# Performance work log

Hardware: AMD Instinct MI355X
Metric: run time of the kernel (lower is better)

Reference implementation:

```python
import jax, jax.numpy as jnp
import numpy as np


def conv2d(x, w, b, stride=1, pad=1):
    y = jax.lax.conv_general_dilated(
        x, w, (stride, stride), [(pad, pad), (pad, pad)],
        dimension_numbers=('NCHW', 'OIHW', 'NCHW'))
    return y + b[None, :, None, None]


def layernorm(x, g, b, eps=1e-5):
    mu = jnp.mean(x, -1, keepdims=True)
    var = jnp.mean((x - mu) ** 2, -1, keepdims=True)
    return (x - mu) * jax.lax.rsqrt(var + eps) * g + b


def setup_inputs() -> dict:
    key = jax.random.key(0)
    ks = iter(jax.random.split(key, 40))
    nf = 4

    def w(shape, scale=0.1):
        return (jax.random.normal(next(ks), shape, jnp.float32) * scale)

    inp = {}
    inp['x'] = jax.random.uniform(next(ks), (8, 3, 512, 512), jnp.float32)
    # curve-estimation convs (channel=4)
    inp['c1_w'], inp['c1_b'] = w((nf, 1, 3, 3)), w((nf,))
    inp['c2_w'], inp['c2_b'] = w((nf, nf, 3, 3)), w((nf,))
    inp['c3_w'], inp['c3_b'] = w((nf, nf, 3, 3)), w((nf,))
    inp['c4_w'], inp['c4_b'] = w((nf, nf, 3, 3)), w((nf,))
    inp['c5_w'], inp['c5_b'] = w((nf, 2 * nf, 3, 3)), w((nf,))
    inp['c6_w'], inp['c6_b'] = w((nf, 2 * nf, 3, 3)), w((nf,))
    inp['c7_w'], inp['c7_b'] = w((1, 2 * nf, 3, 3)), w((1,))
    # global branch: conv 1->16 stride 2, instance norm (affine)
    inp['m_w'], inp['m_b'] = w((16, 1, 3, 3)), w((16,))
    inp['in_g'] = jnp.ones((16,), jnp.float32)
    inp['in_b'] = jnp.zeros((16,), jnp.float32)
    # TF block (d_model=16, nhead=8, dim_ff=128), eval mode (no dropout)
    inp['attn_w'], inp['attn_b'] = w((48, 16)), w((48,))
    inp['out_w'], inp['out_b'] = w((16, 16)), w((16,))
    inp['l1_w'], inp['l1_b'] = w((128, 16)), w((128,))
    inp['l2_w'], inp['l2_b'] = w((16, 128)), w((16,))
    inp['n1_g'] = jnp.ones((16,), jnp.float32)
    inp['n1_b'] = jnp.zeros((16,), jnp.float32)
    inp['n2_g'] = jnp.ones((16,), jnp.float32)
    inp['n2_b'] = jnp.zeros((16,), jnp.float32)
    # F: Conv2d(16, 2, kernel=16, pad=0) over 16x16 -> [B,2,1,1]
    inp['f_w'], inp['f_b'] = w((2, 16, 16, 16)), w((2,))
    return inp


def _forward(x, c1_w, c1_b, c2_w, c2_b, c3_w, c3_b, c4_w, c4_b, c5_w, c5_b,
             c6_w, c6_b, c7_w, c7_b, m_w, m_b, in_g, in_b, attn_w, attn_b,
             out_w, out_b, l1_w, l1_b, l2_w, l2_b, n1_g, n1_b, n2_g, n2_b,
             f_w, f_b):
    relu = jax.nn.relu
    B, _, H, W = x.shape
    red, green, blue = x[:, 0:1], x[:, 1:2], x[:, 2:3]
    v = (red + green + blue) / 3.0  # [B,1,H,W]

    # curve-estimation branch
    x1 = relu(conv2d(v, c1_w, c1_b))
    x2 = relu(conv2d(x1, c2_w, c2_b))
    x3 = relu(conv2d(x2, c3_w, c3_b))
    x4 = relu(conv2d(x3, c4_w, c4_b))
    x5 = relu(conv2d(jnp.concatenate([x3, x4], 1), c5_w, c5_b))
    x6 = relu(conv2d(jnp.concatenate([x2, x5], 1), c6_w, c6_b))
    v_r = jax.nn.sigmoid(conv2d(jnp.concatenate([x1, x6], 1), c7_w, c7_b))

    # where(v>0.999999, 0.999999, .) ; where(v<1e-6, 1e-6, .)  == clip
    v0 = jnp.clip(v, 1e-6, 0.999999)

    # nearest-neighbor resize to 32x32 (torch 'nearest': floor(i * src/dst))
    idx_h = (jnp.arange(32) * H) // 32
    idx_w = (jnp.arange(32) * W) // 32
    v32 = v[:, :, idx_h][:, :, :, idx_w]  # [B,1,32,32]

    # model: conv stride2 -> leaky relu -> instance norm (affine)
    h = conv2d(v32, m_w, m_b, stride=2, pad=1)  # [B,16,16,16]
    h = jnp.where(h >= 0, h, 0.2 * h)
    mu = jnp.mean(h, (2, 3), keepdims=True)
    var = jnp.mean((h - mu) ** 2, (2, 3), keepdims=True)
    v1 = (h - mu) * jax.lax.rsqrt(var + 1e-5)
    v1 = v1 * in_g[None, :, None, None] + in_b[None, :, None, None]

    # TF block on [S=256, B, E=16] tokens, 8 heads of dim 2, eval mode
    bb, cc, ww, hh = v1.shape
    src = v1.reshape(bb, cc, ww * hh).transpose(2, 0, 1)  # [S,B,E]
    S, E, nH = ww * hh, cc, 8
    hd = E // nH
    qkv = src @ attn_w.T + attn_b  # [S,B,3E]
    q, k, vv = jnp.split(qkv, 3, axis=-1)
    q = q.reshape(S, bb, nH, hd)
    k = k.reshape(S, bb, nH, hd)
    vv = vv.reshape(S, bb, nH, hd)
    scores = jnp.einsum('sbhd,tbhd->bhst', q, k) / np.sqrt(hd).astype(np.float32)
    attn = jax.nn.softmax(scores, axis=-1)
    o = jnp.einsum('bhst,tbhd->sbhd', attn, vv).reshape(S, bb, E)
    o = o @ out_w.T + out_b
    src = layernorm(src + o, n1_g, n1_b)
    ff = jax.nn.relu(src @ l1_w.T + l1_b) @ l2_w.T + l2_b
    src = layernorm(src + ff, n2_g, n2_b)
    v5 = src.transpose(1, 2, 0).reshape(bb, cc, ww, hh)

    level = jax.nn.sigmoid(conv2d(v5, f_w, f_b, stride=1, pad=0))[:, :, 0, 0]  # [B,2]

    # per-sample exponent / threshold broadcast (vectorized .item() loop)
    g = (0.1 * level[:, 0] + 0.2)[:, None, None, None]   # [B,1,1,1]
    bcf = (0.04 * level[:, 1] + 0.06)[:, None, None, None]
    r0 = jnp.power(g, v_r)           # g ** r, elementwise per sample
    ev0 = jnp.power(v0, r0)
    L = 400.0 * (bcf - v) ** 3
    L = jnp.where(L < 1e-5, 1e-6, L)
    ev = ev0 - L
    vd = v + 1e-6
    enhance = jnp.concatenate([red / vd * ev, green / vd * ev, blue / vd * ev], 1)
    vvv = jnp.concatenate([v, v, v], 1)
    t = jnp.where(vvv > 0.04, jnp.zeros_like(enhance), enhance)
    return enhance, v_r, t


def reference(x, c1_w, c1_b, c2_w, c2_b, c3_w, c3_b, c4_w, c4_b, c5_w, c5_b,
              c6_w, c6_b, c7_w, c7_b, m_w, m_b, in_g, in_b, attn_w, attn_b,
              out_w, out_b, l1_w, l1_b, l2_w, l2_b, n1_g, n1_b, n2_g, n2_b,
              f_w, f_b):
    return _forward(x, c1_w, c1_b, c2_w, c2_b, c3_w, c3_b, c4_w, c4_b,
                    c5_w, c5_b, c6_w, c6_b, c7_w, c7_b, m_w, m_b, in_g, in_b,
                    attn_w, attn_b, out_w, out_b, l1_w, l1_b, l2_w, l2_b,
                    n1_g, n1_b, n2_g, n2_b, f_w, f_b)
```

## Files before the change

kernel.cpp:

```cpp
#include <hip/hip_runtime.h>
#include <math.h>

#define H 512
#define W 512
#define PLANE (H*W)
#define PLANE4 (PLANE/4)

typedef unsigned int uint;
typedef unsigned short ushort;
typedef _Float16 h2 __attribute__((ext_vector_type(2)));

__device__ __forceinline__ h2 bch2(uint u){ return __builtin_bit_cast(h2, u); }
__device__ __forceinline__ uint pkf16(float a, float b){
  return __builtin_bit_cast(uint, __builtin_amdgcn_cvt_pkrtz(a, b));
}

#define LOADWIN_EVEN(WIN, TL, S, YB, XB) { \
  _Pragma("unroll") for (int r_=0;r_<4;++r_){ \
    uint4 Ua = *(const uint4*)&(TL)[(((YB)+r_)*(S)+(XB))*4]; \
    uint4 Ub = *(const uint4*)&(TL)[(((YB)+r_)*(S)+(XB)+2)*4]; \
    WIN[r_][0][0]=bch2(Ua.x); WIN[r_][0][1]=bch2(Ua.y); \
    WIN[r_][1][0]=bch2(Ua.z); WIN[r_][1][1]=bch2(Ua.w); \
    WIN[r_][2][0]=bch2(Ub.x); WIN[r_][2][1]=bch2(Ub.y); \
    WIN[r_][3][0]=bch2(Ub.z); WIN[r_][3][1]=bch2(Ub.w); } }

#define LOADWIN_ODD(WIN, TL, S, YB, XB) { \
  _Pragma("unroll") for (int r_=0;r_<4;++r_){ \
    uint2 U0 = *(const uint2*)&(TL)[(((YB)+r_)*(S)+(XB))*4]; \
    uint4 U1 = *(const uint4*)&(TL)[(((YB)+r_)*(S)+(XB)+1)*4]; \
    uint2 U2 = *(const uint2*)&(TL)[(((YB)+r_)*(S)+(XB)+3)*4]; \
    WIN[r_][0][0]=bch2(U0.x); WIN[r_][0][1]=bch2(U0.y); \
    WIN[r_][1][0]=bch2(U1.x); WIN[r_][1][1]=bch2(U1.y); \
    WIN[r_][2][0]=bch2(U1.z); WIN[r_][2][1]=bch2(U1.w); \
    WIN[r_][3][0]=bch2(U2.x); WIN[r_][3][1]=bch2(U2.y); } }

#define DOTACC(WIN, WPK, NPTOT, PBASE, NPWIN) { \
  _Pragma("unroll") for (int p_=0;p_<NPWIN;++p_){ \
    _Pragma("unroll") for (int dy_=0;dy_<3;++dy_){ \
      _Pragma("unroll") for (int dx_=0;dx_<3;++dx_){ \
        h2 aa=WIN[dy_][dx_][p_],   bb=WIN[dy_][dx_+1][p_]; \
        h2 cc=WIN[dy_+1][dx_][p_], dd=WIN[dy_+1][dx_+1][p_]; \
        _Pragma("unroll") for (int co_=0;co_<4;++co_){ \
          h2 wv = bch2((WPK)[((co_*(NPTOT))+(PBASE)+p_)*9+dy_*3+dx_]); \
          a00[co_]=__builtin_amdgcn_fdot2(aa,wv,a00[co_],false); \
          a01[co_]=__builtin_amdgcn_fdot2(bb,wv,a01[co_],false); \
          a10[co_]=__builtin_amdgcn_fdot2(cc,wv,a10[co_],false); \
          a11[co_]=__builtin_amdgcn_fdot2(dd,wv,a11[co_],false); } } } } }

#define DOTACC1(WIN, WPK, PBASE) { \
  _Pragma("unroll") for (int p_=0;p_<2;++p_){ \
    _Pragma("unroll") for (int dy_=0;dy_<3;++dy_){ \
      _Pragma("unroll") for (int dx_=0;dx_<3;++dx_){ \
        h2 wv = bch2((WPK)[((PBASE)+p_)*9+dy_*3+dx_]); \
        s00=__builtin_amdgcn_fdot2(WIN[dy_][dx_][p_],  wv,s00,false); \
        s01=__builtin_amdgcn_fdot2(WIN[dy_][dx_+1][p_],wv,s01,false); \
        s10=__builtin_amdgcn_fdot2(WIN[dy_+1][dx_][p_],  wv,s10,false); \
        s11=__builtin_amdgcn_fdot2(WIN[dy_+1][dx_+1][p_],wv,s11,false); } } } }

#define STORE_TILE(TL, S, GOFF) { \
    bool okr0=(unsigned)(gy0+(GOFF)+y0  )<512u; \
    bool okr1=(unsigned)(gy0+(GOFF)+y0+1)<512u; \
    bool okc0=(unsigned)(gx0+(GOFF)+x0  )<512u; \
    bool okc1=(unsigned)(gx0+(GOFF)+x0+1)<512u; \
    float v00[4],v01[4],v10[4],v11[4]; \
    _Pragma("unroll") \
    for (int co_=0;co_<4;++co_){ \
      v00[co_]=(okr0&okc0)?fmaxf(a00[co_],0.f):0.f; \
      v01[co_]=(okr0&okc1)?fmaxf(a01[co_],0.f):0.f; \
      v10[co_]=(okr1&okc0)?fmaxf(a10[co_],0.f):0.f; \
      v11[co_]=(okr1&okc1)?fmaxf(a11[co_],0.f):0.f; } \
    uint4 rowlo, rowhi; \
    rowlo.x=pkf16(v00[0],v00[1]); rowlo.y=pkf16(v00[2],v00[3]); \
    rowlo.z=pkf16(v01[0],v01[1]); rowlo.w=pkf16(v01[2],v01[3]); \
    rowhi.x=pkf16(v10[0],v10[1]); rowhi.y=pkf16(v10[2],v10[3]); \
    rowhi.z=pkf16(v11[0],v11[1]); rowhi.w=pkf16(v11[2],v11[3]); \
    *(uint4*)&(TL)[(y0*(S)+x0)*4]=rowlo; \
    *(uint4*)&(TL)[((y0+1)*(S)+x0)*4]=rowhi; }

template<int S>
__device__ __forceinline__ void accp4sc(const ushort* __restrict__ pl,
    const float* __restrict__ w, int YB, int XB,
    float* a00, float* a01, float* a10, float* a11)
{
  float q[4][4];
  #pragma unroll
  for (int r=0;r<4;++r){
    const ushort* rp = pl + (YB+r)*S + XB;
    h2 p0 = bch2(*(const uint*)rp);
    h2 p1 = bch2(*(const uint*)(rp+2));
    q[r][0]=(float)p0.x; q[r][1]=(float)p0.y; q[r][2]=(float)p1.x; q[r][3]=(float)p1.y;
  }
  #pragma unroll
  for (int dy=0; dy<3; ++dy)
    #pragma unroll
    for (int dx=0; dx<3; ++dx){
      float q00=q[dy][dx], q01=q[dy][dx+1], q10=q[dy+1][dx], q11=q[dy+1][dx+1];
      #pragma unroll
      for (int co=0; co<4; ++co){
        float wv=w[co*9+dy*3+dx];
        a00[co]+=q00*wv; a01[co]+=q01*wv; a10[co]+=q10*wv; a11[co]+=q11*wv;
      }
    }
}

__global__ void k_wprep(const float* __restrict__ c2w, const float* __restrict__ c3w,
                        const float* __restrict__ c4w, const float* __restrict__ c5w,
                        const float* __restrict__ c6w, const float* __restrict__ c7w,
                        uint* __restrict__ wpk){
  for (int i=threadIdx.x; i<540; i+=512){
    const float* src; int INC, rel;
    if (i<72){src=c2w;INC=4;rel=i;}
    else if (i<144){src=c3w;INC=4;rel=i-72;}
    else if (i<216){src=c4w;INC=4;rel=i-144;}
    else if (i<360){src=c5w;INC=8;rel=i-216;}
    else if (i<504){src=c6w;INC=8;rel=i-360;}
    else {src=c7w;INC=8;rel=i-504;}
    int NP=INC/2;
    int co=rel/(NP*9); int r2=rel-co*NP*9; int p=r2/9; int tap=r2-p*9;
    float f0 = src[(co*INC + 2*p  )*9 + tap];
    float f1 = src[(co*INC + 2*p+1)*9 + tap];
    wpk[i] = pkf16(f0, f1);
  }
}

__launch_bounds__(512,2)
__global__ void k_megaconv(const float* __restrict__ xg,
    const float* __restrict__ c1w, const float* __restrict__ c1b,
    const float* __restrict__ c2b, const float* __restrict__ c3b,
    const float* __restrict__ c4b, const float* __restrict__ c5b,
    const float* __restrict__ c6b, const float* __restrict__ c7b,
    const uint* __restrict__ wpk,
    float* __restrict__ vr)
{
  __shared__ __align__(16) ushort vb[46*46];
  __shared__ __align__(16) ushort t1[44*44*4];
  __shared__ __align__(16) ushort t2[42*42*4];
  __shared__ __align__(16) ushort t3[40*40*4];
  __shared__ __align__(16) ushort t4[38*38*4];
  __shared__ __align__(16) ushort t5[36*36*4];
  __shared__ __align__(16) ushort t6[34*34*4];
  int wg=blockIdx.x, b=wg>>8, t=wg&255, ty=t>>4, tx=t&15;
  int gy0=ty*32, gx0=tx*32, tid=threadIdx.x;
  const float* xp = xg + (size_t)b*3*PLANE;

  for (int i=tid;i<46*46;i+=512){
    int rr=i/46, cc=i-rr*46;
    int gy=gy0-7+rr, gx=gx0-7+cc;
    float val=0.f;
    if (((unsigned)gy<512u)&((unsigned)gx<512u)){
      int off=gy*W+gx;
      val=(xp[off]+xp[PLANE+off]+xp[2*PLANE+off])*(1.f/3.f);
    }
    _Float16 hv=(_Float16)val;
    vb[i]=*(ushort*)&hv;
  }
  __syncthreads();

  if (tid < 484){
    int qy=tid/22, qx=tid-qy*22, y0=2*qy, x0=2*qx;
    float a00[4],a01[4],a10[4],a11[4];
    #pragma unroll
    for (int co=0;co<4;++co){ float bv=c1b[co]; a00[co]=bv;a01[co]=bv;a10[co]=bv;a11[co]=bv; }
    accp4sc<46>(vb, c1w, y0, x0, a00,a01,a10,a11);
    STORE_TILE(t1, 44, -6)
  }
  __syncthreads();

  if (tid < 441){
    int qy=tid/21, qx=tid-qy*21, y0=2*qy, x0=2*qx;
    float a00[4],a01[4],a10[4],a11[4];
    #pragma unroll
    for (int co=0;co<4;++co){ float bv=c2b[co]; a00[co]=bv;a01[co]=bv;a10[co]=bv;a11[co]=bv; }
    h2 win[4][4][2];
    LOADWIN_EVEN(win, t1, 44, y0, x0)
    DOTACC(win, wpk+0, 2, 0, 2)
    STORE_TILE(t2, 42, -5)
  }
  __syncthreads();

  if (tid < 400){
    int qy=tid/20, qx=tid-qy*20, y0=2*qy, x0=2*qx;
    float a00[4],a01[4],a10[4],a11[4];
    #pragma unroll
    for (int co=0;co<4;++co){ float bv=c3b[co]; a00[co]=bv;a01[co]=bv;a10[co]=bv;a11[co]=bv; }
    h2 win[4][4][2];
    LOADWIN_EVEN(win, t2, 42, y0, x0)
    DOTACC(win, wpk+72, 2, 0, 2)
    STORE_TILE(t3, 40, -4)
  }
  __syncthreads();

  if (tid < 361){
    int qy=tid/19, qx=tid-qy*19, y0=2*qy, x0=2*qx;
    float a00[4],a01[4],a10[4],a11[4];
    #pragma unroll
    for (int co=0;co<4;++co){ float bv=c4b[co]; a00[co]=bv;a01[co]=bv;a10[co]=bv;a11[co]=bv; }
    h2 win[4][4][2];
    LOADWIN_EVEN(win, t3, 40, y0, x0)
    DOTACC(win, wpk+144, 2, 0, 2)
    STORE_TILE(t4, 38, -3)
  }
  __syncthreads();

  if (tid < 324){
    int qy=tid/18, qx=tid-qy*18, y0=2*qy, x0=2*qx;
    float a00[4],a01[4],a10[4],a11[4];
    #pragma unroll
    for (int co=0;co<4;++co){ float bv=c5b[co]; a00[co]=bv;a01[co]=bv;a10[co]=bv;a11[co]=bv; }
    {
      h2 win[4][4][2];
      LOADWIN_ODD(win, t3, 40, y0+1, x0+1)
      DOTACC(win, wpk+216, 4, 0, 2)
    }
    {
      h2 win[4][4][2];
      LOADWIN_EVEN(win, t4, 38, y0, x0)
      DOTACC(win, wpk+216, 4, 2, 2)
    }
    STORE_TILE(t5, 36, -2)
  }
  __syncthreads();

  if (tid < 289){
    int qy=tid/17, qx=tid-qy*17, y0=2*qy, x0=2*qx;
    float a00[4],a01[4],a10[4],a11[4];
    #pragma unroll
    for (int co=0;co<4;++co){ float bv=c6b[co]; a00[co]=bv;a01[co]=bv;a10[co]=bv;a11[co]=bv; }
    {
      h2 win[4][4][2];
      LOADWIN_ODD(win, t2, 42, y0+3, x0+3)
      DOTACC(win, wpk+360, 4, 0, 2)
    }
    {
      h2 win[4][4][2];
      LOADWIN_EVEN(win, t5, 36, y0, x0)
      DOTACC(win, wpk+360, 4, 2, 2)
    }
    STORE_TILE(t6, 34, -1)
  }
  __syncthreads();

  if (tid < 256){
    int qy=tid>>4, qx=tid&15, y0=2*qy, x0=2*qx;
    float bv=c7b[0];
    float s00=bv, s01=bv, s10=bv, s11=bv;
    {
      h2 win[4][4][2];
      LOADWIN_ODD(win, t1, 44, y0+5, x0+5)
      DOTACC1(win, wpk+504, 0)
    }
    {
      h2 win[4][4][2];
      LOADWIN_EVEN(win, t6, 34, y0, x0)
      DOTACC1(win, wpk+504, 2)
    }
    float* vo = vr + (size_t)b*PLANE;
    *(float2*)&vo[(gy0+y0  )*512 + gx0+x0] =
        make_float2(1.f/(1.f+expf(-s00)), 1.f/(1.f+expf(-s01)));
    *(float2*)&vo[(gy0+y0+1)*512 + gx0+x0] =
        make_float2(1.f/(1.f+expf(-s10)), 1.f/(1.f+expf(-s11)));
  }
}

__launch_bounds__(256)
__global__ void k_mnorm(const float* __restrict__ xg, const float* __restrict__ mw,
                        const float* __restrict__ mb, const float* __restrict__ ing,
                        const float* __restrict__ inb, float* __restrict__ src){
  int bc = blockIdx.x;
  int b = bc >> 4, c = bc & 15;
  int tid = threadIdx.x;
  int i = tid >> 4, j = tid & 15;
  const float* xp = xg + (size_t)b*3*PLANE;
  float s = mb[c];
  #pragma unroll
  for (int dy=0; dy<3; ++dy){
    int ii = 2*i - 1 + dy;
    if ((unsigned)ii >= 32u) continue;
    #pragma unroll
    for (int dx=0; dx<3; ++dx){
      int jj = 2*j - 1 + dx;
      if ((unsigned)jj >= 32u) continue;
      int off = (ii*16)*W + jj*16;
      float vv = (xp[off] + xp[PLANE+off] + xp[2*PLANE+off]) * (1.f/3.f);
      s += vv * mw[c*9 + dy*3 + dx];
    }
  }
  float h = (s >= 0.f) ? s : 0.2f*s;
  __shared__ float red[256];
  red[tid] = h; __syncthreads();
  for (int off=128; off; off>>=1){ if (tid<off) red[tid]+=red[tid+off]; __syncthreads(); }
  float mu = red[0] * (1.f/256.f);
  __syncthreads();
  float d = h - mu;
  red[tid] = d*d; __syncthreads();
  for (int off=128; off; off>>=1){ if (tid<off) red[tid]+=red[tid+off]; __syncthreads(); }
  float var = red[0] * (1.f/256.f);
  float yv = d * rsqrtf(var + 1e-5f) * ing[c] + inb[c];
  src[(size_t)tid*128 + b*16 + c] = yv;
}

__launch_bounds__(256)
__global__ void k_qkv(const float* __restrict__ src, const float* __restrict__ aw,
                      const float* __restrict__ ab, float* __restrict__ qkv){
  int id = blockIdx.x*256 + threadIdx.x;
  int tok = id / 48, o = id % 48;
  const float* sr = src + tok*16;
  float s = ab[o];
  #pragma unroll
  for (int e=0; e<16; ++e) s += sr[e]*aw[o*16+e];
  qkv[tok*48+o] = s;
}

__launch_bounds__(256)
__global__ void k_attn(const float* __restrict__ qkv, float* __restrict__ obuf){
  int b = blockIdx.x >> 3, hh = blockIdx.x & 7;
  int t = threadIdx.x;
  __shared__ float kk0[256], kk1[256], vv0[256], vv1[256];
  int tok = t*8 + b;
  const float* qr = qkv + tok*48;
  kk0[t] = qr[16 + hh*2]; kk1[t] = qr[16 + hh*2 + 1];
  vv0[t] = qr[32 + hh*2]; vv1[t] = qr[32 + hh*2 + 1];
  float q0 = qr[hh*2], q1 = qr[hh*2 + 1];
  __syncthreads();
  const float sc = 0.70710678118654752f;
  float m = -1e30f;
  for (int u=0; u<256; ++u){
    float s = (q0*kk0[u] + q1*kk1[u]) * sc;
    m = fmaxf(m, s);
  }
  float l = 0.f, a0 = 0.f, a1 = 0.f;
  for (int u=0; u<256; ++u){
    float s = (q0*kk0[u] + q1*kk1[u]) * sc;
    float p = expf(s - m);
    l += p; a0 += p*vv0[u]; a1 += p*vv1[u];
  }
  float inv = 1.f/l;
  obuf[tok*16 + hh*2]     = a0*inv;
  obuf[tok*16 + hh*2 + 1] = a1*inv;
}

__launch_bounds__(256)
__global__ void k_oproj_ln(const float* __restrict__ obuf, const float* __restrict__ ow,
                           const float* __restrict__ obias, const float* __restrict__ g,
                           const float* __restrict__ bb, float* __restrict__ src){
  int tok = blockIdx.x*256 + threadIdx.x;
  const float* orow = obuf + tok*16;
  float xv[16];
  #pragma unroll
  for (int e=0; e<16; ++e){
    float s = obias[e];
    #pragma unroll
    for (int f=0; f<16; ++f) s += orow[f]*ow[e*16+f];
    xv[e] = src[tok*16+e] + s;
  }
  float mu = 0.f;
  #pragma unroll
  for (int e=0; e<16; ++e) mu += xv[e];
  mu *= (1.f/16.f);
  float var = 0.f;
  #pragma unroll
  for (int e=0; e<16; ++e){ float d = xv[e]-mu; var += d*d; }
  var *= (1.f/16.f);
  float rs = rsqrtf(var + 1e-5f);
  #pragma unroll
  for (int e=0; e<16; ++e) src[tok*16+e] = (xv[e]-mu)*rs*g[e] + bb[e];
}

__launch_bounds__(64)
__global__ void k_ffn_ln(float* __restrict__ src, const float* __restrict__ w1,
                         const float* __restrict__ b1, const float* __restrict__ w2,
                         const float* __restrict__ b2, const float* __restrict__ g,
                         const float* __restrict__ bb){
  int tok = blockIdx.x;
  int tid = threadIdx.x;
  __shared__ float srow[16], h1[128], xr[16];
  if (tid < 16) srow[tid] = src[tok*16+tid];
  __syncthreads();
  for (int i = tid; i < 128; i += 64){
    float s = b1[i];
    #pragma unroll
    for (int e=0; e<16; ++e) s += srow[e]*w1[i*16+e];
    h1[i] = fmaxf(s, 0.f);
  }
  __syncthreads();
  if (tid < 16){
    float s = b2[tid];
    for (int j=0; j<128; ++j) s += h1[j]*w2[tid*128+j];
    xr[tid] = srow[tid] + s;
  }
  __syncthreads();
  if (tid < 16){
    float mu = 0.f;
    #pragma unroll
    for (int e=0; e<16; ++e) mu += xr[e];
    mu *= (1.f/16.f);
    float var = 0.f;
    #pragma unroll
    for (int e=0; e<16; ++e){ float d = xr[e]-mu; var += d*d; }
    var *= (1.f/16.f);
    src[tok*16+tid] = (xr[tid]-mu)*rsqrtf(var+1e-5f)*g[tid] + bb[tid];
  }
}

__launch_bounds__(256)
__global__ void k_level(const float* __restrict__ src, const float* __restrict__ fw,
                        const float* __restrict__ fb, float* __restrict__ gb){
  int b = blockIdx.x >> 1, k = blockIdx.x & 1;
  int tid = threadIdx.x;
  float s = 0.f;
  #pragma unroll
  for (int c=0; c<16; ++c)
    s += src[(size_t)tid*128 + b*16 + c] * fw[(k*16+c)*256 + tid];
  __shared__ float red[256];
  red[tid] = s; __syncthreads();
  for (int off=128; off; off>>=1){ if (tid<off) red[tid]+=red[tid+off]; __syncthreads(); }
  if (tid == 0){
    float lev = 1.f/(1.f + expf(-(red[0] + fb[k])));
    gb[b*2+k] = (k==0) ? (0.1f*lev + 0.2f) : (0.04f*lev + 0.06f);
  }
}

__launch_bounds__(256)
__global__ void k_final(const float* __restrict__ x, const float* __restrict__ gb,
                        float* __restrict__ out){
  int id = blockIdx.x*256 + threadIdx.x;
  int b = id >> 16, p = id & 65535;
  const float4* xr = (const float4*)(x + (size_t)(b*3+0)*PLANE);
  const float4* xg = (const float4*)(x + (size_t)(b*3+1)*PLANE);
  const float4* xb = (const float4*)(x + (size_t)(b*3+2)*PLANE);
  const float4* vrp = (const float4*)(out + 6291456 + (size_t)b*PLANE);
  float4 R = xr[p], G = xg[p], Bl = xb[p], VR = vrp[p];
  float gg = gb[b*2+0], bc = gb[b*2+1];
  float lg = log2f(gg);
  float4 er, eg, eb, tr, tg, tb;
#define COMP(SUF, RF, GF, BF, VRF) {            \
    float vv = (RF + GF + BF)/3.f;              \
    float v0 = fminf(fmaxf(vv, 1e-6f), 0.999999f); \
    float r0 = exp2f(VRF * lg);                 \
    float ev0 = exp2f(r0 * log2f(v0));          \
    float d = bc - vv;                          \
    float L = 400.f*d*d*d;                      \
    L = (L < 1e-5f) ? 1e-6f : L;                \
    float fac = (ev0 - L) / (vv + 1e-6f);       \
    er.SUF = RF*fac; eg.SUF = GF*fac; eb.SUF = BF*fac; \
    bool z = vv > 0.04f;                        \
    tr.SUF = z ? 0.f : er.SUF; tg.SUF = z ? 0.f : eg.SUF; tb.SUF = z ? 0.f : eb.SUF; }
  COMP(x, R.x, G.x, Bl.x, VR.x)
  COMP(y, R.y, G.y, Bl.y, VR.y)
  COMP(z, R.z, G.z, Bl.z, VR.z)
  COMP(w, R.w, G.w, Bl.w, VR.w)
#undef COMP
  float4* oe = (float4*)out;
  float4* ot = (float4*)(out + 8388608);
  oe[(size_t)(b*3+0)*PLANE4 + p] = er;
  oe[(size_t)(b*3+1)*PLANE4 + p] = eg;
  oe[(size_t)(b*3+2)*PLANE4 + p] = eb;
  ot[(size_t)(b*3+0)*PLANE4 + p] = tr;
  ot[(size_t)(b*3+1)*PLANE4 + p] = tg;
  ot[(size_t)(b*3+2)*PLANE4 + p] = tb;
}

extern "C" void kernel_launch(void* const* d_in, const int* in_sizes, int n_in,
                              void* d_out, int out_size, void* d_ws, size_t ws_size,
                              hipStream_t stream) {
  const float* x    = (const float*)d_in[0];
  const float* c1w  = (const float*)d_in[1];  const float* c1b = (const float*)d_in[2];
  const float* c2w  = (const float*)d_in[3];  const float* c2b = (const float*)d_in[4];
  const float* c3w  = (const float*)d_in[5];  const float* c3b = (const float*)d_in[6];
  const float* c4w  = (const float*)d_in[7];  const float* c4b = (const float*)d_in[8];
  const float* c5w  = (const float*)d_in[9];  const float* c5b = (const float*)d_in[10];
  const float* c6w  = (const float*)d_in[11]; const float* c6b = (const float*)d_in[12];
  const float* c7w  = (const float*)d_in[13]; const float* c7b = (const float*)d_in[14];
  const float* mw   = (const float*)d_in[15]; const float* mb  = (const float*)d_in[16];
  const float* ing  = (const float*)d_in[17]; const float* inb = (const float*)d_in[18];
  const float* aw   = (const float*)d_in[19]; const float* ab  = (const float*)d_in[20];
  const float* ow   = (const float*)d_in[21]; const float* ob  = (const float*)d_in[22];
  const float* l1w  = (const float*)d_in[23]; const float* l1b = (const float*)d_in[24];
  const float* l2w  = (const float*)d_in[25]; const float* l2b = (const float*)d_in[26];
  const float* n1g  = (const float*)d_in[27]; const float* n1b = (const float*)d_in[28];
  const float* n2g  = (const float*)d_in[29]; const float* n2b = (const float*)d_in[30];
  const float* fw   = (const float*)d_in[31]; const float* fb  = (const float*)d_in[32];

  uint* wpk = (uint*)d_ws;
  float* smallws = (float*)(wpk + 1024);
  float* src  = smallws;
  float* qkv  = src + 32768;
  float* obuf = qkv + 98304;
  float* gb   = obuf+ 32768;
  float* out  = (float*)d_out;
  float* vr   = out + 6291456;

  k_wprep<<<1,512,0,stream>>>(c2w, c3w, c4w, c5w, c6w, c7w, wpk);
  k_megaconv<<<2048,512,0,stream>>>(x, c1w, c1b, c2b, c3b, c4b, c5b, c6b, c7b,
                                    wpk, vr);
  k_mnorm<<<128,256,0,stream>>>(x, mw, mb, ing, inb, src);
  k_qkv<<<384,256,0,stream>>>(src, aw, ab, qkv);
  k_attn<<<64,256,0,stream>>>(qkv, obuf);
  k_oproj_ln<<<8,256,0,stream>>>(obuf, ow, ob, n1g, n1b, src);
  k_ffn_ln<<<2048,64,0,stream>>>(src, l1w, l1b, l2w, l2b, n2g, n2b);
  k_level<<<16,256,0,stream>>>(src, fw, fb, gb);
  k_final<<<2048,256,0,stream>>>(x, gb, out);
}
```

Baseline: 167.3 us.

## Fuse transformer branch into one kernel and fold final enhancement into megaconv

The global branch (instance norm, QKV, attention, out-projection with layernorm, FFN with layernorm, level head) was six small kernels. It is now one kernel, `k_small`, with one block per batch and all intermediates kept in shared memory; attention also drops the running-max subtraction. That kernel now runs before the conv kernel, so the conv epilogue can apply the curve enhancement directly and write both outputs. This removes the separate final pass over the image and the extra re-read of the stored v_r map, plus several launches. The cost is that the small branch now runs serially on only 8 blocks before the big conv kernel, and the conv epilogue gets heavier.

```diff
diff --git a/kernel.cpp b/kernel.cpp
--- a/kernel.cpp
+++ b/kernel.cpp
@@ -123,14 +123,190 @@
   }
 }
 
+__launch_bounds__(256)
+__global__ void k_small(const float* __restrict__ xg,
+    const float* __restrict__ mw, const float* __restrict__ mb,
+    const float* __restrict__ ing, const float* __restrict__ inb,
+    const float* __restrict__ aw, const float* __restrict__ ab,
+    const float* __restrict__ ow, const float* __restrict__ ob,
+    const float* __restrict__ l1w, const float* __restrict__ l1b,
+    const float* __restrict__ l2w, const float* __restrict__ l2b,
+    const float* __restrict__ n1g, const float* __restrict__ n1b,
+    const float* __restrict__ n2g, const float* __restrict__ n2b,
+    const float* __restrict__ fw, const float* __restrict__ fb,
+    float* __restrict__ gb)
+{
+  __shared__ float srcl[256][17];
+  __shared__ float qkvl[256][49];
+  __shared__ float obufl[256][17];
+  __shared__ float red[512];
+  __shared__ float musig[32];
+  int b = blockIdx.x, tid = threadIdx.x;
+  int i = tid>>4, j = tid&15;
+  const float* xp = xg + (size_t)b*3*PLANE;
+
+  float vs[3][3];
+  #pragma unroll
+  for (int dy=0;dy<3;++dy){
+    int ii = 2*i-1+dy;
+    #pragma unroll
+    for (int dx=0;dx<3;++dx){
+      int jj = 2*j-1+dx;
+      float v = 0.f;
+      if (((unsigned)ii<32u)&((unsigned)jj<32u)){
+        int off = (ii*16)*W + jj*16;
+        v = (xp[off]+xp[PLANE+off]+xp[2*PLANE+off])*(1.f/3.f);
+      }
+      vs[dy][dx]=v;
+    }
+  }
+  float h[16];
+  #pragma unroll
+  for (int c=0;c<16;++c){
+    float s = mb[c];
+    #pragma unroll
+    for (int dy=0;dy<3;++dy)
+      #pragma unroll
+      for (int dx=0;dx<3;++dx) s += vs[dy][dx]*mw[c*9+dy*3+dx];
+    h[c] = (s>=0.f)?s:0.2f*s;
+    srcl[tid][c]=h[c];
+  }
+  __syncthreads();
+  {
+    int c = tid>>4, g = tid&15;
+    float s1=0.f, s2=0.f;
+    #pragma unroll
+    for (int p=0;p<16;++p){ float v=srcl[g*16+p][c]; s1+=v; s2+=v*v; }
+    red[c*16+g]=s1; red[256+c*16+g]=s2;
+  }
+  __syncthreads();
+  if (tid<16){
+    float S1=0.f,S2=0.f;
+    #pragma unroll
+    for (int g=0;g<16;++g){ S1+=red[tid*16+g]; S2+=red[256+tid*16+g]; }
+    float mu=S1*(1.f/256.f);
+    float var=S2*(1.f/256.f)-mu*mu;
+    musig[tid]=mu; musig[16+tid]=rsqrtf(var+1e-5f);
+  }
+  __syncthreads();
+  #pragma unroll
+  for (int c=0;c<16;++c)
+    srcl[tid][c] = (h[c]-musig[c])*musig[16+c]*ing[c]+inb[c];
+  __syncthreads();
+
+  {
+    float s[16];
+    #pragma unroll
+    for (int e=0;e<16;++e) s[e]=srcl[tid][e];
+    for (int o=0;o<48;++o){
+      float t = ab[o];
+      #pragma unroll
+      for (int e=0;e<16;++e) t += s[e]*aw[o*16+e];
+      qkvl[tid][o]=t;
+    }
+  }
+  __syncthreads();
+
+  {
+    const float sc = 0.70710678118654752f;
+    #pragma unroll
+    for (int hh=0;hh<8;++hh){
+      float q0=qkvl[tid][2*hh], q1=qkvl[tid][2*hh+1];
+      float l=0.f,a0=0.f,a1=0.f;
+      for (int u=0;u<256;++u){
+        float k0=qkvl[u][16+2*hh], k1=qkvl[u][16+2*hh+1];
+        float p=expf((q0*k0+q1*k1)*sc);
+        l+=p; a0+=p*qkvl[u][32+2*hh]; a1+=p*qkvl[u][32+2*hh+1];
+      }
+      float inv=1.f/l;
+      obufl[tid][2*hh]=a0*inv; obufl[tid][2*hh+1]=a1*inv;
+    }
+  }
+  __syncthreads();
+
+  {
+    float xv[16];
+    #pragma unroll
+    for (int e=0;e<16;++e){
+      float t=ob[e];
+      #pragma unroll
+      for (int f=0;f<16;++f) t += obufl[tid][f]*ow[e*16+f];
+      xv[e]=srcl[tid][e]+t;
+    }
+    float mu=0.f;
+    #pragma unroll
+    for (int e=0;e<16;++e) mu+=xv[e];
+    mu*=(1.f/16.f);
+    float var=0.f;
+    #pragma unroll
+    for (int e=0;e<16;++e){ float d=xv[e]-mu; var+=d*d; }
+    var*=(1.f/16.f);
+    float rs=rsqrtf(var+1e-5f);
+    #pragma unroll
+    for (int e=0;e<16;++e) srcl[tid][e]=(xv[e]-mu)*rs*n1g[e]+n1b[e];
+  }
+  __syncthreads();
+
+  {
+    float s[16], x2[16];
+    #pragma unroll
+    for (int e=0;e<16;++e){ s[e]=srcl[tid][e]; x2[e]=l2b[e]; }
+    for (int ii2=0;ii2<128;++ii2){
+      float t=l1b[ii2];
+      #pragma unroll
+      for (int e=0;e<16;++e) t += s[e]*l1w[ii2*16+e];
+      t = fmaxf(t,0.f);
+      #pragma unroll
+      for (int e=0;e<16;++e) x2[e] += t*l2w[e*128+ii2];
+    }
+    float xv[16];
+    #pragma unroll
+    for (int e=0;e<16;++e) xv[e]=s[e]+x2[e];
+    float mu=0.f;
+    #pragma unroll
+    for (int e=0;e<16;++e) mu+=xv[e];
+    mu*=(1.f/16.f);
+    float var=0.f;
+    #pragma unroll
+    for (int e=0;e<16;++e){ float d=xv[e]-mu; var+=d*d; }
+    var*=(1.f/16.f);
+    float rs=rsqrtf(var+1e-5f);
+    #pragma unroll
+    for (int e=0;e<16;++e) srcl[tid][e]=(xv[e]-mu)*rs*n2g[e]+n2b[e];
+  }
+  __syncthreads();
+
+  {
+    float p0=0.f,p1=0.f;
+    #pragma unroll
+    for (int c=0;c<16;++c){
+      float sv=srcl[tid][c];
+      p0 += sv*fw[c*256+tid];
+      p1 += sv*fw[(16+c)*256+tid];
+    }
+    red[tid]=p0; red[256+tid]=p1;
+  }
+  __syncthreads();
+  for (int off=128; off; off>>=1){
+    if (tid<off){ red[tid]+=red[tid+off]; red[256+tid]+=red[256+tid+off]; }
+    __syncthreads();
+  }
+  if (tid==0){
+    float lev0 = 1.f/(1.f+expf(-(red[0]+fb[0])));
+    float lev1 = 1.f/(1.f+expf(-(red[256]+fb[1])));
+    gb[b*2+0] = 0.1f*lev0+0.2f;
+    gb[b*2+1] = 0.04f*lev1+0.06f;
+  }
+}
+
 __launch_bounds__(512,2)
 __global__ void k_megaconv(const float* __restrict__ xg,
     const float* __restrict__ c1w, const float* __restrict__ c1b,
     const float* __restrict__ c2b, const float* __restrict__ c3b,
     const float* __restrict__ c4b, const float* __restrict__ c5b,
     const float* __restrict__ c6b, const float* __restrict__ c7b,
-    const uint* __restrict__ wpk,
-    float* __restrict__ vr)
+    const uint* __restrict__ wpk, const float* __restrict__ gb2,
+    float* __restrict__ out)
 {
   __shared__ __align__(16) ushort vb[46*46];
   __shared__ __align__(16) ushort t1[44*44*4];
@@ -254,210 +430,46 @@
       LOADWIN_EVEN(win, t6, 34, y0, x0)
       DOTACC1(win, wpk+504, 2)
     }
-    float* vo = vr + (size_t)b*PLANE;
-    *(float2*)&vo[(gy0+y0  )*512 + gx0+x0] =
-        make_float2(1.f/(1.f+expf(-s00)), 1.f/(1.f+expf(-s01)));
-    *(float2*)&vo[(gy0+y0+1)*512 + gx0+x0] =
-        make_float2(1.f/(1.f+expf(-s10)), 1.f/(1.f+expf(-s11)));
-  }
-}
-
-__launch_bounds__(256)
-__global__ void k_mnorm(const float* __restrict__ xg, const float* __restrict__ mw,
-                        const float* __restrict__ mb, const float* __restrict__ ing,
-                        const float* __restrict__ inb, float* __restrict__ src){
-  int bc = blockIdx.x;
-  int b = bc >> 4, c = bc & 15;
-  int tid = threadIdx.x;
-  int i = tid >> 4, j = tid & 15;
-  const float* xp = xg + (size_t)b*3*PLANE;
-  float s = mb[c];
-  #pragma unroll
-  for (int dy=0; dy<3; ++dy){
-    int ii = 2*i - 1 + dy;
-    if ((unsigned)ii >= 32u) continue;
-    #pragma unroll
-    for (int dx=0; dx<3; ++dx){
-      int jj = 2*j - 1 + dx;
-      if ((unsigned)jj >= 32u) continue;
-      int off = (ii*16)*W + jj*16;
-      float vv = (xp[off] + xp[PLANE+off] + xp[2*PLANE+off]) * (1.f/3.f);
-      s += vv * mw[c*9 + dy*3 + dx];
-    }
-  }
-  float h = (s >= 0.f) ? s : 0.2f*s;
-  __shared__ float red[256];
-  red[tid] = h; __syncthreads();
-  for (int off=128; off; off>>=1){ if (tid<off) red[tid]+=red[tid+off]; __syncthreads(); }
-  float mu = red[0] * (1.f/256.f);
-  __syncthreads();
-  float d = h - mu;
-  red[tid] = d*d; __syncthreads();
-  for (int off=128; off; off>>=1){ if (tid<off) red[tid]+=red[tid+off]; __syncthreads(); }
-  float var = red[0] * (1.f/256.f);
-  float yv = d * rsqrtf(var + 1e-5f) * ing[c] + inb[c];
-  src[(size_t)tid*128 + b*16 + c] = yv;
-}
-
-__launch_bounds__(256)
-__global__ void k_qkv(const float* __restrict__ src, const float* __restrict__ aw,
-                      const float* __restrict__ ab, float* __restrict__ qkv){
-  int id = blockIdx.x*256 + threadIdx.x;
-  int tok = id / 48, o = id % 48;
-  const float* sr = src + tok*16;
-  float s = ab[o];
-  #pragma unroll
-  for (int e=0; e<16; ++e) s += sr[e]*aw[o*16+e];
-  qkv[tok*48+o] = s;
-}
-
-__launch_bounds__(256)
-__global__ void k_attn(const float* __restrict__ qkv, float* __restrict__ obuf){
-  int b = blockIdx.x >> 3, hh = blockIdx.x & 7;
-  int t = threadIdx.x;
-  __shared__ float kk0[256], kk1[256], vv0[256], vv1[256];
-  int tok = t*8 + b;
-  const float* qr = qkv + tok*48;
-  kk0[t] = qr[16 + hh*2]; kk1[t] = qr[16 + hh*2 + 1];
-  vv0[t] = qr[32 + hh*2]; vv1[t] = qr[32 + hh*2 + 1];
-  float q0 = qr[hh*2], q1 = qr[hh*2 + 1];
-  __syncthreads();
-  const float sc = 0.70710678118654752f;
-  float m = -1e30f;
-  for (int u=0; u<256; ++u){
-    float s = (q0*kk0[u] + q1*kk1[u]) * sc;
-    m = fmaxf(m, s);
-  }
-  float l = 0.f, a0 = 0.f, a1 = 0.f;
-  for (int u=0; u<256; ++u){
-    float s = (q0*kk0[u] + q1*kk1[u]) * sc;
-    float p = expf(s - m);
-    l += p; a0 += p*vv0[u]; a1 += p*vv1[u];
-  }
-  float inv = 1.f/l;
-  obuf[tok*16 + hh*2]     = a0*inv;
-  obuf[tok*16 + hh*2 + 1] = a1*inv;
-}
-
-__launch_bounds__(256)
-__global__ void k_oproj_ln(const float* __restrict__ obuf, const float* __restrict__ ow,
-                           const float* __restrict__ obias, const float* __restrict__ g,
-                           const float* __restrict__ bb, float* __restrict__ src){
-  int tok = blockIdx.x*256 + threadIdx.x;
-  const float* orow = obuf + tok*16;
-  float xv[16];
-  #pragma unroll
-  for (int e=0; e<16; ++e){
-    float s = obias[e];
-    #pragma unroll
-    for (int f=0; f<16; ++f) s += orow[f]*ow[e*16+f];
-    xv[e] = src[tok*16+e] + s;
-  }
-  float mu = 0.f;
-  #pragma unroll
-  for (int e=0; e<16; ++e) mu += xv[e];
-  mu *= (1.f/16.f);
-  float var = 0.f;
-  #pragma unroll
-  for (int e=0; e<16; ++e){ float d = xv[e]-mu; var += d*d; }
-  var *= (1.f/16.f);
-  float rs = rsqrtf(var + 1e-5f);
-  #pragma unroll
-  for (int e=0; e<16; ++e) src[tok*16+e] = (xv[e]-mu)*rs*g[e] + bb[e];
-}
-
-__launch_bounds__(64)
-__global__ void k_ffn_ln(float* __restrict__ src, const float* __restrict__ w1,
-                         const float* __restrict__ b1, const float* __restrict__ w2,
-                         const float* __restrict__ b2, const float* __restrict__ g,
-                         const float* __restrict__ bb){
-  int tok = blockIdx.x;
-  int tid = threadIdx.x;
-  __shared__ float srow[16], h1[128], xr[16];
-  if (tid < 16) srow[tid] = src[tok*16+tid];
-  __syncthreads();
-  for (int i = tid; i < 128; i += 64){
-    float s = b1[i];
-    #pragma unroll
-    for (int e=0; e<16; ++e) s += srow[e]*w1[i*16+e];
-    h1[i] = fmaxf(s, 0.f);
-  }
-  __syncthreads();
-  if (tid < 16){
-    float s = b2[tid];
-    for (int j=0; j<128; ++j) s += h1[j]*w2[tid*128+j];
-    xr[tid] = srow[tid] + s;
-  }
-  __syncthreads();
-  if (tid < 16){
-    float mu = 0.f;
-    #pragma unroll
-    for (int e=0; e<16; ++e) mu += xr[e];
-    mu *= (1.f/16.f);
-    float var = 0.f;
-    #pragma unroll
-    for (int e=0; e<16; ++e){ float d = xr[e]-mu; var += d*d; }
-    var *= (1.f/16.f);
-    src[tok*16+tid] = (xr[tid]-mu)*rsqrtf(var+1e-5f)*g[tid] + bb[tid];
-  }
-}
-
-__launch_bounds__(256)
-__global__ void k_level(const float* __restrict__ src, const float* __restrict__ fw,
-                        const float* __restrict__ fb, float* __restrict__ gb){
-  int b = blockIdx.x >> 1, k = blockIdx.x & 1;
-  int tid = threadIdx.x;
-  float s = 0.f;
-  #pragma unroll
-  for (int c=0; c<16; ++c)
-    s += src[(size_t)tid*128 + b*16 + c] * fw[(k*16+c)*256 + tid];
-  __shared__ float red[256];
-  red[tid] = s; __syncthreads();
-  for (int off=128; off; off>>=1){ if (tid<off) red[tid]+=red[tid+off]; __syncthreads(); }
-  if (tid == 0){
-    float lev = 1.f/(1.f + expf(-(red[0] + fb[k])));
-    gb[b*2+k] = (k==0) ? (0.1f*lev + 0.2f) : (0.04f*lev + 0.06f);
-  }
-}
-
-__launch_bounds__(256)
-__global__ void k_final(const float* __restrict__ x, const float* __restrict__ gb,
-                        float* __restrict__ out){
-  int id = blockIdx.x*256 + threadIdx.x;
-  int b = id >> 16, p = id & 65535;
-  const float4* xr = (const float4*)(x + (size_t)(b*3+0)*PLANE);
-  const float4* xg = (const float4*)(x + (size_t)(b*3+1)*PLANE);
-  const float4* xb = (const float4*)(x + (size_t)(b*3+2)*PLANE);
-  const float4* vrp = (const float4*)(out + 6291456 + (size_t)b*PLANE);
-  float4 R = xr[p], G = xg[p], Bl = xb[p], VR = vrp[p];
-  float gg = gb[b*2+0], bc = gb[b*2+1];
-  float lg = log2f(gg);
-  float4 er, eg, eb, tr, tg, tb;
-#define COMP(SUF, RF, GF, BF, VRF) {            \
-    float vv = (RF + GF + BF)/3.f;              \
-    float v0 = fminf(fmaxf(vv, 1e-6f), 0.999999f); \
-    float r0 = exp2f(VRF * lg);                 \
-    float ev0 = exp2f(r0 * log2f(v0));          \
-    float d = bc - vv;                          \
-    float L = 400.f*d*d*d;                      \
-    L = (L < 1e-5f) ? 1e-6f : L;                \
-    float fac = (ev0 - L) / (vv + 1e-6f);       \
-    er.SUF = RF*fac; eg.SUF = GF*fac; eb.SUF = BF*fac; \
-    bool z = vv > 0.04f;                        \
-    tr.SUF = z ? 0.f : er.SUF; tg.SUF = z ? 0.f : eg.SUF; tb.SUF = z ? 0.f : eb.SUF; }
-  COMP(x, R.x, G.x, Bl.x, VR.x)
-  COMP(y, R.y, G.y, Bl.y, VR.y)
-  COMP(z, R.z, G.z, Bl.z, VR.z)
-  COMP(w, R.w, G.w, Bl.w, VR.w)
-#undef COMP
-  float4* oe = (float4*)out;
-  float4* ot = (float4*)(out + 8388608);
-  oe[(size_t)(b*3+0)*PLANE4 + p] = er;
-  oe[(size_t)(b*3+1)*PLANE4 + p] = eg;
-  oe[(size_t)(b*3+2)*PLANE4 + p] = eb;
-  ot[(size_t)(b*3+0)*PLANE4 + p] = tr;
-  ot[(size_t)(b*3+1)*PLANE4 + p] = tg;
-  ot[(size_t)(b*3+2)*PLANE4 + p] = tb;
+    s00 = 1.f/(1.f+expf(-s00)); s01 = 1.f/(1.f+expf(-s01));
+    s10 = 1.f/(1.f+expf(-s10)); s11 = 1.f/(1.f+expf(-s11));
+    float* vo = out + 6291456 + (size_t)b*PLANE;
+    *(float2*)&vo[(gy0+y0  )*512 + gx0+x0] = make_float2(s00,s01);
+    *(float2*)&vo[(gy0+y0+1)*512 + gx0+x0] = make_float2(s10,s11);
+
+    float gg = gb2[b*2+0], bcf = gb2[b*2+1];
+    float lg = log2f(gg);
+    #pragma unroll
+    for (int py=0; py<2; ++py){
+      int gy=gy0+y0+py, gx=gx0+x0;
+      int off=gy*W+gx;
+      float2 R = *(const float2*)&xp[off];
+      float2 G = *(const float2*)&xp[PLANE+off];
+      float2 B = *(const float2*)&xp[2*PLANE+off];
+      float vr0 = py? s10:s00, vr1 = py? s11:s01;
+      float2 er,eg,eb,tr,tg,tb;
+#define COMP1(RF,GF,BF,VRF,ER,EG,EB,TR,TG,TB) { \
+      float vv=(RF+GF+BF)*(1.f/3.f); \
+      float v0c=fminf(fmaxf(vv,1e-6f),0.999999f); \
+      float r0=exp2f((VRF)*lg); \
+      float ev0=exp2f(r0*log2f(v0c)); \
+      float dd=bcf-vv; \
+      float L=400.f*dd*dd*dd; \
+      L=(L<1e-5f)?1e-6f:L; \
+      float fac=(ev0-L)/(vv+1e-6f); \
+      ER=RF*fac; EG=GF*fac; EB=BF*fac; \
+      bool z=vv>0.04f; \
+      TR=z?0.f:ER; TG=z?0.f:EG; TB=z?0.f:EB; }
+      COMP1(R.x,G.x,B.x,vr0, er.x,eg.x,eb.x, tr.x,tg.x,tb.x)
+      COMP1(R.y,G.y,B.y,vr1, er.y,eg.y,eb.y, tr.y,tg.y,tb.y)
+#undef COMP1
+      *(float2*)&out[(size_t)(b*3+0)*PLANE + off] = er;
+      *(float2*)&out[(size_t)(b*3+1)*PLANE + off] = eg;
+      *(float2*)&out[(size_t)(b*3+2)*PLANE + off] = eb;
+      *(float2*)&out[8388608 + (size_t)(b*3+0)*PLANE + off] = tr;
+      *(float2*)&out[8388608 + (size_t)(b*3+1)*PLANE + off] = tg;
+      *(float2*)&out[8388608 + (size_t)(b*3+2)*PLANE + off] = tb;
+    }
+  }
 }
 
 extern "C" void kernel_launch(void* const* d_in, const int* in_sizes, int n_in,
@@ -482,22 +494,13 @@
   const float* fw   = (const float*)d_in[31]; const float* fb  = (const float*)d_in[32];
 
   uint* wpk = (uint*)d_ws;
-  float* smallws = (float*)(wpk + 1024);
-  float* src  = smallws;
-  float* qkv  = src + 32768;
-  float* obuf = qkv + 98304;
-  float* gb   = obuf+ 32768;
+  float* gb = (float*)(wpk + 1024);
   float* out  = (float*)d_out;
-  float* vr   = out + 6291456;
 
   k_wprep<<<1,512,0,stream>>>(c2w, c3w, c4w, c5w, c6w, c7w, wpk);
+  k_small<<<8,256,0,stream>>>(x, mw, mb, ing, inb, aw, ab, ow, ob,
+                              l1w, l1b, l2w, l2b, n1g, n1b, n2g, n2b,
+                              fw, fb, gb);
   k_megaconv<<<2048,512,0,stream>>>(x, c1w, c1b, c2b, c3b, c4b, c5b, c6b, c7b,
-                                    wpk, vr);
-  k_mnorm<<<128,256,0,stream>>>(x, mw, mb, ing, inb, src);
-  k_qkv<<<384,256,0,stream>>>(src, aw, ab, qkv);
-  k_attn<<<64,256,0,stream>>>(qkv, obuf);
-  k_oproj_ln<<<8,256,0,stream>>>(obuf, ow, ob, n1g, n1b, src);
-  k_ffn_ln<<<2048,64,0,stream>>>(src, l1w, l1b, l2w, l2b, n2g, n2b);
-  k_level<<<16,256,0,stream>>>(src, fw, fb, gb);
-  k_final<<<2048,256,0,stream>>>(x, gb, out);
+                                    wpk, gb, out);
 }
```

New measurement: 276.5 us. +65.2%, slower.
